# Kernel optimization log

Hardware: AMD Instinct MI355X
Metric: run time of the kernel (lower is better)

The kernel has to match this reference:

```python
import jax, jax.numpy as jnp
import numpy as np

N_KERNELS = 11
B, Q, D, E, C = 128, 32, 512, 300, 128

def _kernel_mus(n):
    mus = [1.0]
    bs = 2.0 / (n - 1)
    mus.append(1 - bs / 2)
    for i in range(1, n - 1):
        mus.append(mus[i] - bs)
    return np.array(mus, dtype=np.float32)

def _kernel_sigmas(n):
    bs = 2.0 / (n - 1)
    return np.array([0.001] + [0.5 * bs] * (n - 1), dtype=np.float32)

def setup_inputs():
    key = jax.random.key(0)
    ks = jax.random.split(key, 10)
    return {
        "query_embeddings": jax.random.normal(ks[0], (B, Q, E), jnp.float32),
        "document_embeddings": jax.random.normal(ks[1], (B, D, E), jnp.float32),
        "query_pad_oov_mask": jnp.ones((B, Q), jnp.float32),
        "document_pad_oov_mask": jnp.ones((B, D), jnp.float32),
        "conv1_w": jax.random.normal(ks[2], (C, E, 1), jnp.float32) * 0.05,
        "conv1_b": jnp.zeros((C,), jnp.float32),
        "conv2_w": jax.random.normal(ks[3], (C, E, 2), jnp.float32) * 0.05,
        "conv2_b": jnp.zeros((C,), jnp.float32),
        "conv3_w": jax.random.normal(ks[4], (C, E, 3), jnp.float32) * 0.05,
        "conv3_b": jnp.zeros((C,), jnp.float32),
        "nn_scaler": jnp.full((1,), 0.01, jnp.float32),
        "dense_w": jax.random.uniform(ks[5], (1, N_KERNELS * 9), jnp.float32, -0.014, 0.014),
        "dense_b": jnp.zeros((1,), jnp.float32),
        "dense_mean_w": jax.random.normal(ks[6], (1, N_KERNELS * 9), jnp.float32) * 0.05,
        "dense_mean_b": jnp.zeros((1,), jnp.float32),
        "dense_comb_w": jax.random.normal(ks[7], (1, 2), jnp.float32) * 0.5,
    }

def _conv_relu(x, w, b):
    # x: [B, L, E] -> [B, L, C]; right-pad by k-1 (ConstantPad1d((0, k-1))) so out len == L
    k = w.shape[-1]
    y = jax.lax.conv_general_dilated(x.transpose(0, 2, 1), w, (1,), [(0, k - 1)],
                                     dimension_numbers=("NCH", "OIH", "NCH"))
    return jax.nn.relu(y + b[None, :, None]).transpose(0, 2, 1)

def _kernel_pool(q, d, qd_mask, q_mask, doc_len, mu, sigma, scaler):
    # cosine matrix (AllenNLP CosineMatrixAttention: L2-normalize with 1e-13 tie-break)
    qn = q / (jnp.linalg.norm(q, axis=-1, keepdims=True) + 1e-13)
    dn = d / (jnp.linalg.norm(d, axis=-1, keepdims=True) + 1e-13)
    cos = jnp.einsum("bqc,bdc->bqd", qn, dn) * qd_mask
    # RBF soft-histogram kernels over the similarity matrix: [B,q,d,K]
    kr = jnp.exp(-(cos[..., None] - mu) ** 2 / (2.0 * sigma ** 2)) * qd_mask[..., None]
    pkq = kr.sum(axis=2)  # [B, Q, K]
    std = (jnp.log(jnp.clip(pkq, 1e-10)) * scaler * q_mask[..., None]).sum(axis=1)
    pkq_mean = pkq / doc_len[:, None, None]
    mean = (jnp.log(jnp.clip(pkq_mean, 1e-10)) * scaler * q_mask[..., None]).sum(axis=1)
    return std, mean

def _forward(qe, de, qm, dm, c1w, c1b, c2w, c2b, c3w, c3b, ns, dw, db, dmw, dmb, dcw):
    mu = jnp.asarray(_kernel_mus(N_KERNELS))
    sigma = jnp.asarray(_kernel_sigmas(N_KERNELS))
    qd_mask = qm[:, :, None] * dm[:, None, :]
    doc_len = dm.sum(axis=1)
    convs = [(c1w, c1b), (c2w, c2b), (c3w, c3b)]
    q_res = [_conv_relu(qe, w, b) for w, b in convs]
    d_res = [_conv_relu(de, w, b) for w, b in convs]
    std_list, mean_list = [], []
    for qr in q_res:
        for dr in d_res:
            s, m = _kernel_pool(qr, dr, qd_mask, qm, doc_len, mu, sigma, ns)
            std_list.append(s)
            mean_list.append(m)
    all_grams = jnp.concatenate(std_list, axis=1)       # [B, 9*K]
    all_grams_mean = jnp.concatenate(mean_list, axis=1)
    dense_out = all_grams @ dw.T + db
    dense_mean_out = all_grams_mean @ dmw.T + dmb
    comb = jnp.concatenate([dense_out, dense_mean_out], axis=1) @ dcw.T
    return comb[:, 0]

def reference(query_embeddings, document_embeddings, query_pad_oov_mask, document_pad_oov_mask,
              conv1_w, conv1_b, conv2_w, conv2_b, conv3_w, conv3_b,
              nn_scaler, dense_w, dense_b, dense_mean_w, dense_mean_b, dense_comb_w):
    return _forward(query_embeddings, document_embeddings, query_pad_oov_mask, document_pad_oov_mask,
                    conv1_w, conv1_b, conv2_w, conv2_b, conv3_w, conv3_b,
                    nn_scaler, dense_w, dense_b, dense_mean_w, dense_mean_b, dense_comb_w)
```

## Files before the change

kernel.cpp:

```cpp
#include <hip/hip_runtime.h>
#include <hip/hip_bf16.h>
#include <cstdint>

namespace {

typedef __bf16 bf8v __attribute__((ext_vector_type(8)));
typedef __bf16 bf4v __attribute__((ext_vector_type(4)));
typedef float  f4v  __attribute__((ext_vector_type(4)));
typedef uint32_t u32x4 __attribute__((ext_vector_type(4)));

constexpr int kB = 128;
constexpr int kQ = 32;
constexpr int kD = 512;
constexpr int kE = 300;
constexpr int kC = 128;
constexpr int kK = 11;

constexpr size_t QNB_B = 491520;
constexpr size_t DNB_B = 3637248;
constexpr size_t PKQ_B = 53968896;

constexpr float LOG2E = 1.4426950408889634f;

constexpr int XS_STRIDE = 336;

__global__ __launch_bounds__(256) void prep_kernel(
    const float* __restrict__ w1, const float* __restrict__ w2, const float* __restrict__ w3,
    __bf16* __restrict__ wb)
{
  int i = blockIdx.x * 256 + threadIdx.x;
  if (i >= 245760) return;
  int el = i & 31;
  int sc = i >> 5;
  int c  = sc & 127;
  int chunk = sc >> 7;
  int slab = chunk / 10;
  int ks = chunk - slab * 10;
  int e = ks * 32 + el;
  float v = 0.f;
  if (e < kE) {
    if (slab == 0)      v = w1[c * kE + e];
    else if (slab <= 2) v = w2[(c * kE + e) * 2 + (slab - 1)];
    else                v = w3[(c * kE + e) * 3 + (slab - 3)];
  }
  wb[i] = (__bf16)v;
}

template<int VM>
__device__ __forceinline__ void wait_vm() {
  if constexpr (VM == 4) asm volatile("s_waitcnt vmcnt(4)" ::: "memory");
  else                   asm volatile("s_waitcnt vmcnt(0)" ::: "memory");
  __builtin_amdgcn_sched_barrier(0);
}

__device__ __forceinline__ void issue4(u32x4 (&Wset)[4], const __bf16* p) {
  asm volatile("global_load_dwordx4 %0, %1, off"             : "=v"(Wset[0]) : "v"(p) : "memory");
  asm volatile("global_load_dwordx4 %0, %1, off offset:1024" : "=v"(Wset[1]) : "v"(p) : "memory");
  asm volatile("global_load_dwordx4 %0, %1, off offset:2048" : "=v"(Wset[2]) : "v"(p) : "memory");
  asm volatile("global_load_dwordx4 %0, %1, off offset:3072" : "=v"(Wset[3]) : "v"(p) : "memory");
}

__device__ __forceinline__ void mfma8(bf8v A0, bf8v A1, u32x4 (&Ws)[4], f4v (&acc)[2][4]) {
  #pragma unroll
  for (int nf = 0; nf < 4; ++nf) {
    bf8v Wf = __builtin_bit_cast(bf8v, Ws[nf]);
    acc[0][nf] = __builtin_amdgcn_mfma_f32_16x16x32_bf16(A0, Wf, acc[0][nf], 0, 0, 0);
    acc[1][nf] = __builtin_amdgcn_mfma_f32_16x16x32_bf16(A1, Wf, acc[1][nf], 0, 0, 0);
  }
}

template<int NJ, int CH0>
__device__ __forceinline__ void conv_grp(
    const __bf16* __restrict__ wb, const __bf16* __restrict__ Xs,
    int lr, int g, int wm, int wn, f4v (&acc)[2][4])
{
  const __bf16* wl = wb + (size_t)CH0 * 4096 + (wn * 64 + lr) * 32 + g * 8;
  const int arow = wm * 32 + lr;
  const int ae = g * 8;

  u32x4 W0[4], W1[4];
  issue4(W0, wl);
  issue4(W1, wl + 4096);
  const __bf16* wnext = wl + 2 * 4096;

  #pragma unroll
  for (int j = 0; j < NJ; ++j) {
    const __bf16* xr = Xs + (size_t)(arow + j) * XS_STRIDE + ae;
    const int nks = (j == NJ - 1) ? 8 : 10;
    #pragma unroll 1
    for (int ks = 0; ks < nks; ks += 2) {
      bf8v A0 = *(const bf8v*)(xr + ks * 32);
      bf8v A1 = *(const bf8v*)(xr + 16 * XS_STRIDE + ks * 32);
      wait_vm<4>();
      mfma8(A0, A1, W0, acc);
      issue4(W0, wnext); wnext += 4096;
      bf8v B0 = *(const bf8v*)(xr + ks * 32 + 32);
      bf8v B1 = *(const bf8v*)(xr + 16 * XS_STRIDE + ks * 32 + 32);
      wait_vm<4>();
      mfma8(B0, B1, W1, acc);
      issue4(W1, wnext); wnext += 4096;
    }
  }
  const __bf16* xr = Xs + (size_t)(arow + NJ - 1) * XS_STRIDE + ae;
  bf8v A0 = *(const bf8v*)(xr + 8 * 32);
  bf8v A1 = *(const bf8v*)(xr + 16 * XS_STRIDE + 8 * 32);
  wait_vm<4>();
  mfma8(A0, A1, W0, acc);
  bf8v B0 = *(const bf8v*)(xr + 9 * 32);
  bf8v B1 = *(const bf8v*)(xr + 16 * XS_STRIDE + 9 * 32);
  wait_vm<0>();
  mfma8(B0, B1, W1, acc);
}

__global__ __launch_bounds__(256, 3) void conv_fused(
    const float* __restrict__ qe, const float* __restrict__ de,
    const __bf16* __restrict__ wb,
    const float* __restrict__ b1, const float* __restrict__ b2, const float* __restrict__ b3,
    __bf16* __restrict__ qnb, __bf16* __restrict__ dnb)
{
  const int bx = blockIdx.x;
  const int b  = blockIdx.y;
  const bool isq = (bx == 0);
  const int L  = isq ? kQ : kD;
  const int p0 = isq ? 0 : (bx - 1) * 64;
  const float* xsrc = (isq ? qe : de) + (size_t)b * L * kE;

  const int t = threadIdx.x;
  const int w = t >> 6, l = t & 63;
  const int wm = w & 1, wn = w >> 1;
  const int lr = l & 15, g = l >> 4;

  __shared__ __align__(16) __bf16 Xs[66 * XS_STRIDE];
  __shared__ float sqs[2][64];

  for (int idx = t; idx < 66 * 82; idx += 256) {
    int row = idx / 82, c4 = idx - row * 82;
    int gp = p0 + row;
    float4 v = make_float4(0.f, 0.f, 0.f, 0.f);
    if (gp < L && c4 < 75) v = *(const float4*)(xsrc + (size_t)gp * kE + c4 * 4);
    bf4v hv = { (__bf16)v.x, (__bf16)v.y, (__bf16)v.z, (__bf16)v.w };
    *(bf4v*)&Xs[row * XS_STRIDE + c4 * 4] = hv;
  }
  __syncthreads();

  #pragma unroll
  for (int grp = 0; grp < 3; ++grp) {
    f4v acc[2][4];
    #pragma unroll
    for (int mf = 0; mf < 2; ++mf)
      #pragma unroll
      for (int nf = 0; nf < 4; ++nf)
        acc[mf][nf] = (f4v)0.f;

    if (grp == 0)      conv_grp<1, 0>(wb, Xs, lr, g, wm, wn, acc);
    else if (grp == 1) conv_grp<2, 10>(wb, Xs, lr, g, wm, wn, acc);
    else               conv_grp<3, 30>(wb, Xs, lr, g, wm, wn, acc);

    const float* bias = (grp == 0) ? b1 : ((grp == 1) ? b2 : b3);
    float bvs[4];
    #pragma unroll
    for (int nf = 0; nf < 4; ++nf) bvs[nf] = bias[wn * 64 + nf * 16 + lr];

    f4v ssum[2];
    #pragma unroll
    for (int mf = 0; mf < 2; ++mf) {
      ssum[mf] = (f4v)0.f;
      #pragma unroll
      for (int nf = 0; nf < 4; ++nf)
        #pragma unroll
        for (int r = 0; r < 4; ++r) {
          float y = fmaxf(acc[mf][nf][r] + bvs[nf], 0.f);
          acc[mf][nf][r] = y;
          ssum[mf][r] += y * y;
        }
    }
    #pragma unroll
    for (int off = 1; off < 16; off <<= 1)
      #pragma unroll
      for (int mf = 0; mf < 2; ++mf)
        #pragma unroll
        for (int r = 0; r < 4; ++r)
          ssum[mf][r] += __shfl_xor(ssum[mf][r], off);

    __syncthreads();
    if (lr == 0) {
      #pragma unroll
      for (int mf = 0; mf < 2; ++mf)
        *(float4*)&sqs[wn][wm * 32 + mf * 16 + g * 4] = *(float4*)&ssum[mf];
    }
    __syncthreads();
    f4v inv[2];
    #pragma unroll
    for (int mf = 0; mf < 2; ++mf) {
      float4 o = *(const float4*)&sqs[1 - wn][wm * 32 + mf * 16 + g * 4];
      inv[mf][0] = 1.f / (sqrtf(ssum[mf][0] + o.x) + 1e-13f);
      inv[mf][1] = 1.f / (sqrtf(ssum[mf][1] + o.y) + 1e-13f);
      inv[mf][2] = 1.f / (sqrtf(ssum[mf][2] + o.z) + 1e-13f);
      inv[mf][3] = 1.f / (sqrtf(ssum[mf][3] + o.w) + 1e-13f);
    }
    __syncthreads();
    __bf16* outp = (isq ? qnb : dnb) + ((size_t)(grp * kB + b)) * L * kC;
    #pragma unroll
    for (int mf = 0; mf < 2; ++mf) {
      #pragma unroll
      for (int r = 0; r < 4; ++r) {
        int gp = p0 + wm * 32 + mf * 16 + g * 4 + r;
        if (gp < L) {
          #pragma unroll
          for (int nf = 0; nf < 4; ++nf) {
            int c = wn * 64 + nf * 16 + lr;
            outp[(size_t)gp * kC + c] = (__bf16)(acc[mf][nf][r] * inv[mf][r]);
          }
        }
      }
    }
  }
}

__global__ __launch_bounds__(256) void pool_mfma(
    const __bf16* __restrict__ qnb,
    const __bf16* __restrict__ dnb,
    const float* __restrict__ qmask,
    const float* __restrict__ dmask,
    float* __restrict__ pkq)
{
  const int pair = blockIdx.x;
  const int b = blockIdx.y;
  const int qi = pair / 3, dj = pair - qi * 3;
  const __bf16* qb = qnb + ((size_t)qi * kB + b) * kQ * kC;
  const __bf16* db = dnb + ((size_t)dj * kB + b) * kD * kC;

  const int t = threadIdx.x;
  const int w = t >> 6, l = t & 63;
  const int lr = l & 15, g = l >> 4;

  __shared__ float red[4][2][16][kK];

  bf8v Bq[2][4];
  #pragma unroll
  for (int qt = 0; qt < 2; ++qt)
    #pragma unroll
    for (int kc = 0; kc < 4; ++kc)
      Bq[qt][kc] = *(const bf8v*)&qb[(size_t)(qt * 16 + lr) * kC + kc * 32 + g * 8];

  float qmv[2];
  #pragma unroll
  for (int qt = 0; qt < 2; ++qt) qmv[qt] = qmask[b * kQ + qt * 16 + lr];

  const float c1[10] = { 129.84255368f, 100.98865286f,  72.13475204f,  43.28085123f,  14.42695041f,
                         -14.42695041f, -43.28085123f, -72.13475204f, -100.98865286f, -129.84255368f };
  const float c2[10] = { -58.42914915f, -35.34602850f, -18.03368801f, -6.49212768f, -0.72134752f,
                          -0.72134752f,  -6.49212768f, -18.03368801f, -35.34602850f, -58.42914915f };
  const float C50 = -50.f * LOG2E;
  const float C0  = -500000.f * LOG2E;

  float pk[2][kK];
  #pragma unroll
  for (int qt = 0; qt < 2; ++qt)
    #pragma unroll
    for (int k = 0; k < kK; ++k) pk[qt][k] = 0.f;

  const int dt0 = w * 8;
  bf8v An[4];
  #pragma unroll
  for (int kc = 0; kc < 4; ++kc)
    An[kc] = *(const bf8v*)&db[(size_t)(dt0 * 16 + lr) * kC + kc * 32 + g * 8];

  for (int dtl = 0; dtl < 8; ++dtl) {
    const int drow0 = (dt0 + dtl) * 16;
    bf8v Ac[4];
    #pragma unroll
    for (int kc = 0; kc < 4; ++kc) Ac[kc] = An[kc];
    if (dtl < 7) {
      #pragma unroll
      for (int kc = 0; kc < 4; ++kc)
        An[kc] = *(const bf8v*)&db[(size_t)(drow0 + 16 + lr) * kC + kc * 32 + g * 8];
    }
    f4v acc0 = (f4v)0.f, acc1 = (f4v)0.f;
    #pragma unroll
    for (int kc = 0; kc < 4; ++kc) {
      acc0 = __builtin_amdgcn_mfma_f32_16x16x32_bf16(Ac[kc], Bq[0][kc], acc0, 0, 0, 0);
      acc1 = __builtin_amdgcn_mfma_f32_16x16x32_bf16(Ac[kc], Bq[1][kc], acc1, 0, 0, 0);
    }
    float4 dmv = *(const float4*)&dmask[b * kD + drow0 + g * 4];
    #pragma unroll
    for (int qt = 0; qt < 2; ++qt) {
      const f4v& a = qt ? acc1 : acc0;
      #pragma unroll
      for (int r = 0; r < 4; ++r) {
        float dm = (r == 0) ? dmv.x : (r == 1) ? dmv.y : (r == 2) ? dmv.z : dmv.w;
        float off = fmaf(dm, 1000.f, -1000.f);
        float s = a[r] * qmv[qt] * dm;
        float s2 = s * s;
        float base = fmaf(s2, C50, off);
        float dd = s - 1.f;
        pk[qt][0] += exp2f(fmaf(dd * dd, C0, off));
        #pragma unroll
        for (int k = 0; k < 10; ++k)
          pk[qt][k + 1] += exp2f(fmaf(c1[k], s, base) + c2[k]);
      }
    }
  }

  #pragma unroll
  for (int off = 16; off < 64; off <<= 1)
    #pragma unroll
    for (int qt = 0; qt < 2; ++qt)
      #pragma unroll
      for (int k = 0; k < kK; ++k)
        pk[qt][k] += __shfl_xor(pk[qt][k], off);

  if (l < 16) {
    #pragma unroll
    for (int qt = 0; qt < 2; ++qt)
      #pragma unroll
      for (int k = 0; k < kK; ++k)
        red[w][qt][lr][k] = pk[qt][k];
  }
  __syncthreads();
  for (int i = t; i < 2 * 16 * kK; i += 256) {
    int qt = i / (16 * kK);
    int rem = i - qt * 16 * kK;
    int lq = rem / kK, k = rem - lq * kK;
    float v = red[0][qt][lq][k] + red[1][qt][lq][k] + red[2][qt][lq][k] + red[3][qt][lq][k];
    int q = qt * 16 + lq;
    pkq[(((size_t)pair * kB + b) * kQ + q) * kK + k] = v * qmask[b * kQ + q];
  }
}

__global__ __launch_bounds__(128) void finalize_kernel(
    const float* __restrict__ pkq, const float* __restrict__ qmask,
    const float* __restrict__ dmask, const float* __restrict__ nsp,
    const float* __restrict__ dw, const float* __restrict__ dbp,
    const float* __restrict__ dmw, const float* __restrict__ dmbp,
    const float* __restrict__ dcw, float* __restrict__ out)
{
  const int b = blockIdx.x;
  const int t = threadIdx.x;
  __shared__ float sh[4];
  float dl = 0.f;
  for (int d = t; d < kD; d += 128) dl += dmask[b * kD + d];
  #pragma unroll
  for (int off = 1; off < 64; off <<= 1) dl += __shfl_xor(dl, off);
  if ((t & 63) == 0) sh[t >> 6] = dl;
  __syncthreads();
  const float idl = 1.f / (sh[0] + sh[1]);
  const float sc = nsp[0];
  float ps = 0.f, pm = 0.f;
  for (int i = t; i < 99; i += 128) {
    int pr = i / kK, kk = i - pr * kK;
    const float* base = pkq + ((size_t)pr * kB + b) * kQ * kK + kk;
    float ss = 0.f, sm = 0.f;
    for (int q = 0; q < kQ; ++q) {
      float v = base[q * kK];
      float qq = qmask[b * kQ + q];
      ss += __logf(fmaxf(v, 1e-10f)) * qq;
      sm += __logf(fmaxf(v * idl, 1e-10f)) * qq;
    }
    ps += dw[i] * ss;
    pm += dmw[i] * sm;
  }
  ps *= sc; pm *= sc;
  #pragma unroll
  for (int off = 1; off < 64; off <<= 1) { ps += __shfl_xor(ps, off); pm += __shfl_xor(pm, off); }
  __syncthreads();
  if ((t & 63) == 0) { sh[t >> 6] = ps; sh[2 + (t >> 6)] = pm; }
  __syncthreads();
  if (t == 0) {
    float PS = sh[0] + sh[1] + dbp[0];
    float PM = sh[2] + sh[3] + dmbp[0];
    out[b] = dcw[0] * PS + dcw[1] * PM;
  }
}

}

extern "C" void kernel_launch(void* const* d_in, const int* in_sizes, int n_in,
                              void* d_out, int out_size, void* d_ws, size_t ws_size,
                              hipStream_t stream) {
  const float* qe  = (const float*)d_in[0];
  const float* de  = (const float*)d_in[1];
  const float* qm  = (const float*)d_in[2];
  const float* dm  = (const float*)d_in[3];
  const float* w1  = (const float*)d_in[4];
  const float* b1  = (const float*)d_in[5];
  const float* w2  = (const float*)d_in[6];
  const float* b2  = (const float*)d_in[7];
  const float* w3  = (const float*)d_in[8];
  const float* b3  = (const float*)d_in[9];
  const float* ns  = (const float*)d_in[10];
  const float* dw  = (const float*)d_in[11];
  const float* db  = (const float*)d_in[12];
  const float* dmw = (const float*)d_in[13];
  const float* dmb = (const float*)d_in[14];
  const float* dcw = (const float*)d_in[15];
  float* out = (float*)d_out;

  char* wsb = (char*)d_ws;
  __bf16* wb  = (__bf16*)wsb;
  __bf16* qnb = (__bf16*)(wsb + QNB_B);
  __bf16* dnb = (__bf16*)(wsb + DNB_B);
  float*  pkq = (float*)(wsb + PKQ_B);

  prep_kernel<<<960, 256, 0, stream>>>(w1, w2, w3, wb);
  conv_fused<<<dim3(9, kB), 256, 0, stream>>>(qe, de, wb, b1, b2, b3, qnb, dnb);
  pool_mfma<<<dim3(9, kB), 256, 0, stream>>>(qnb, dnb, qm, dm, pkq);
  finalize_kernel<<<kB, 128, 0, stream>>>(pkq, qm, dm, ns, dw, db, dmw, dmb, dcw, out);
}
```

Before: 166.8 us.

## Shrink conv tile to 32 positions, staging output through LDS for coalesced stores

The conv block tile shrinks from 64 to 32 sequence positions. The four waves now split the 128 output channels as 4x32 instead of a 2x2 grid, which halves per-wave accumulators and weight registers. The grid grows to 17 blocks per batch and the occupancy hint rises from 3 to 5 blocks per CU. Normalized outputs are staged in an LDS buffer and written as 16-byte coalesced vectors instead of scattered 2-byte stores. In exchange, each block reloads the full weight set for half as many rows, which doubles global weight traffic per output.

```diff
diff --git a/kernel.cpp b/kernel.cpp
--- a/kernel.cpp
+++ b/kernel.cpp
@@ -23,6 +23,7 @@
 constexpr float LOG2E = 1.4426950408889634f;
 
 constexpr int XS_STRIDE = 336;
+constexpr int TB_STRIDE = 136;
 
 __global__ __launch_bounds__(256) void prep_kernel(
     const float* __restrict__ w1, const float* __restrict__ w2, const float* __restrict__ w3,
@@ -48,21 +49,19 @@
 
 template<int VM>
 __device__ __forceinline__ void wait_vm() {
-  if constexpr (VM == 4) asm volatile("s_waitcnt vmcnt(4)" ::: "memory");
+  if constexpr (VM == 2) asm volatile("s_waitcnt vmcnt(2)" ::: "memory");
   else                   asm volatile("s_waitcnt vmcnt(0)" ::: "memory");
   __builtin_amdgcn_sched_barrier(0);
 }
 
-__device__ __forceinline__ void issue4(u32x4 (&Wset)[4], const __bf16* p) {
+__device__ __forceinline__ void issue2(u32x4 (&Wset)[2], const __bf16* p) {
   asm volatile("global_load_dwordx4 %0, %1, off"             : "=v"(Wset[0]) : "v"(p) : "memory");
   asm volatile("global_load_dwordx4 %0, %1, off offset:1024" : "=v"(Wset[1]) : "v"(p) : "memory");
-  asm volatile("global_load_dwordx4 %0, %1, off offset:2048" : "=v"(Wset[2]) : "v"(p) : "memory");
-  asm volatile("global_load_dwordx4 %0, %1, off offset:3072" : "=v"(Wset[3]) : "v"(p) : "memory");
-}
-
-__device__ __forceinline__ void mfma8(bf8v A0, bf8v A1, u32x4 (&Ws)[4], f4v (&acc)[2][4]) {
-  #pragma unroll
-  for (int nf = 0; nf < 4; ++nf) {
+}
+
+__device__ __forceinline__ void mfma4(bf8v A0, bf8v A1, u32x4 (&Ws)[2], f4v (&acc)[2][2]) {
+  #pragma unroll
+  for (int nf = 0; nf < 2; ++nf) {
     bf8v Wf = __builtin_bit_cast(bf8v, Ws[nf]);
     acc[0][nf] = __builtin_amdgcn_mfma_f32_16x16x32_bf16(A0, Wf, acc[0][nf], 0, 0, 0);
     acc[1][nf] = __builtin_amdgcn_mfma_f32_16x16x32_bf16(A1, Wf, acc[1][nf], 0, 0, 0);
@@ -72,47 +71,46 @@
 template<int NJ, int CH0>
 __device__ __forceinline__ void conv_grp(
     const __bf16* __restrict__ wb, const __bf16* __restrict__ Xs,
-    int lr, int g, int wm, int wn, f4v (&acc)[2][4])
+    int w, int lr, int g, f4v (&acc)[2][2])
 {
-  const __bf16* wl = wb + (size_t)CH0 * 4096 + (wn * 64 + lr) * 32 + g * 8;
-  const int arow = wm * 32 + lr;
+  const __bf16* wl = wb + (size_t)CH0 * 4096 + (w * 32 + lr) * 32 + g * 8;
   const int ae = g * 8;
 
-  u32x4 W0[4], W1[4];
-  issue4(W0, wl);
-  issue4(W1, wl + 4096);
+  u32x4 W0[2], W1[2];
+  issue2(W0, wl);
+  issue2(W1, wl + 4096);
   const __bf16* wnext = wl + 2 * 4096;
 
   #pragma unroll
   for (int j = 0; j < NJ; ++j) {
-    const __bf16* xr = Xs + (size_t)(arow + j) * XS_STRIDE + ae;
+    const __bf16* xr = Xs + (size_t)(lr + j) * XS_STRIDE + ae;
     const int nks = (j == NJ - 1) ? 8 : 10;
     #pragma unroll 1
     for (int ks = 0; ks < nks; ks += 2) {
       bf8v A0 = *(const bf8v*)(xr + ks * 32);
       bf8v A1 = *(const bf8v*)(xr + 16 * XS_STRIDE + ks * 32);
-      wait_vm<4>();
-      mfma8(A0, A1, W0, acc);
-      issue4(W0, wnext); wnext += 4096;
+      wait_vm<2>();
+      mfma4(A0, A1, W0, acc);
+      issue2(W0, wnext); wnext += 4096;
       bf8v B0 = *(const bf8v*)(xr + ks * 32 + 32);
       bf8v B1 = *(const bf8v*)(xr + 16 * XS_STRIDE + ks * 32 + 32);
-      wait_vm<4>();
-      mfma8(B0, B1, W1, acc);
-      issue4(W1, wnext); wnext += 4096;
-    }
-  }
-  const __bf16* xr = Xs + (size_t)(arow + NJ - 1) * XS_STRIDE + ae;
+      wait_vm<2>();
+      mfma4(B0, B1, W1, acc);
+      issue2(W1, wnext); wnext += 4096;
+    }
+  }
+  const __bf16* xr = Xs + (size_t)(lr + NJ - 1) * XS_STRIDE + ae;
   bf8v A0 = *(const bf8v*)(xr + 8 * 32);
   bf8v A1 = *(const bf8v*)(xr + 16 * XS_STRIDE + 8 * 32);
-  wait_vm<4>();
-  mfma8(A0, A1, W0, acc);
+  wait_vm<2>();
+  mfma4(A0, A1, W0, acc);
   bf8v B0 = *(const bf8v*)(xr + 9 * 32);
   bf8v B1 = *(const bf8v*)(xr + 16 * XS_STRIDE + 9 * 32);
   wait_vm<0>();
-  mfma8(B0, B1, W1, acc);
-}
-
-__global__ __launch_bounds__(256, 3) void conv_fused(
+  mfma4(B0, B1, W1, acc);
+}
+
+__global__ __launch_bounds__(256, 5) void conv_fused(
     const float* __restrict__ qe, const float* __restrict__ de,
     const __bf16* __restrict__ wb,
     const float* __restrict__ b1, const float* __restrict__ b2, const float* __restrict__ b3,
@@ -122,18 +120,18 @@
   const int b  = blockIdx.y;
   const bool isq = (bx == 0);
   const int L  = isq ? kQ : kD;
-  const int p0 = isq ? 0 : (bx - 1) * 64;
+  const int p0 = isq ? 0 : (bx - 1) * 32;
   const float* xsrc = (isq ? qe : de) + (size_t)b * L * kE;
 
   const int t = threadIdx.x;
   const int w = t >> 6, l = t & 63;
-  const int wm = w & 1, wn = w >> 1;
   const int lr = l & 15, g = l >> 4;
 
-  __shared__ __align__(16) __bf16 Xs[66 * XS_STRIDE];
-  __shared__ float sqs[2][64];
-
-  for (int idx = t; idx < 66 * 82; idx += 256) {
+  __shared__ __align__(16) __bf16 Xs[34 * XS_STRIDE];
+  __shared__ __align__(16) __bf16 tbuf[32 * TB_STRIDE];
+  __shared__ float sqs4[4][32];
+
+  for (int idx = t; idx < 34 * 82; idx += 256) {
     int row = idx / 82, c4 = idx - row * 82;
     int gp = p0 + row;
     float4 v = make_float4(0.f, 0.f, 0.f, 0.f);
@@ -145,28 +143,28 @@
 
   #pragma unroll
   for (int grp = 0; grp < 3; ++grp) {
-    f4v acc[2][4];
+    f4v acc[2][2];
     #pragma unroll
     for (int mf = 0; mf < 2; ++mf)
       #pragma unroll
-      for (int nf = 0; nf < 4; ++nf)
+      for (int nf = 0; nf < 2; ++nf)
         acc[mf][nf] = (f4v)0.f;
 
-    if (grp == 0)      conv_grp<1, 0>(wb, Xs, lr, g, wm, wn, acc);
-    else if (grp == 1) conv_grp<2, 10>(wb, Xs, lr, g, wm, wn, acc);
-    else               conv_grp<3, 30>(wb, Xs, lr, g, wm, wn, acc);
+    if (grp == 0)      conv_grp<1, 0>(wb, Xs, w, lr, g, acc);
+    else if (grp == 1) conv_grp<2, 10>(wb, Xs, w, lr, g, acc);
+    else               conv_grp<3, 30>(wb, Xs, w, lr, g, acc);
 
     const float* bias = (grp == 0) ? b1 : ((grp == 1) ? b2 : b3);
-    float bvs[4];
-    #pragma unroll
-    for (int nf = 0; nf < 4; ++nf) bvs[nf] = bias[wn * 64 + nf * 16 + lr];
+    float bvs[2];
+    #pragma unroll
+    for (int nf = 0; nf < 2; ++nf) bvs[nf] = bias[w * 32 + nf * 16 + lr];
 
     f4v ssum[2];
     #pragma unroll
     for (int mf = 0; mf < 2; ++mf) {
       ssum[mf] = (f4v)0.f;
       #pragma unroll
-      for (int nf = 0; nf < 4; ++nf)
+      for (int nf = 0; nf < 2; ++nf)
         #pragma unroll
         for (int r = 0; r < 4; ++r) {
           float y = fmaxf(acc[mf][nf][r] + bvs[nf], 0.f);
@@ -182,38 +180,40 @@
         for (int r = 0; r < 4; ++r)
           ssum[mf][r] += __shfl_xor(ssum[mf][r], off);
 
+    if (lr == 0) {
+      #pragma unroll
+      for (int mf = 0; mf < 2; ++mf)
+        *(float4*)&sqs4[w][mf * 16 + g * 4] = *(float4*)&ssum[mf];
+    }
     __syncthreads();
-    if (lr == 0) {
-      #pragma unroll
-      for (int mf = 0; mf < 2; ++mf)
-        *(float4*)&sqs[wn][wm * 32 + mf * 16 + g * 4] = *(float4*)&ssum[mf];
-    }
+    float inv[2][4];
+    #pragma unroll
+    for (int mf = 0; mf < 2; ++mf)
+      #pragma unroll
+      for (int r = 0; r < 4; ++r) {
+        int row = mf * 16 + g * 4 + r;
+        float s = sqs4[0][row] + sqs4[1][row] + sqs4[2][row] + sqs4[3][row];
+        inv[mf][r] = 1.f / (sqrtf(s) + 1e-13f);
+      }
+    #pragma unroll
+    for (int mf = 0; mf < 2; ++mf)
+      #pragma unroll
+      for (int nf = 0; nf < 2; ++nf)
+        #pragma unroll
+        for (int r = 0; r < 4; ++r) {
+          int row = mf * 16 + g * 4 + r;
+          int c = w * 32 + nf * 16 + lr;
+          tbuf[row * TB_STRIDE + c] = (__bf16)(acc[mf][nf][r] * inv[mf][r]);
+        }
     __syncthreads();
-    f4v inv[2];
-    #pragma unroll
-    for (int mf = 0; mf < 2; ++mf) {
-      float4 o = *(const float4*)&sqs[1 - wn][wm * 32 + mf * 16 + g * 4];
-      inv[mf][0] = 1.f / (sqrtf(ssum[mf][0] + o.x) + 1e-13f);
-      inv[mf][1] = 1.f / (sqrtf(ssum[mf][1] + o.y) + 1e-13f);
-      inv[mf][2] = 1.f / (sqrtf(ssum[mf][2] + o.z) + 1e-13f);
-      inv[mf][3] = 1.f / (sqrtf(ssum[mf][3] + o.w) + 1e-13f);
-    }
+    __bf16* outp = (isq ? qnb : dnb) + ((size_t)(grp * kB + b)) * L * kC + (size_t)p0 * kC;
+    #pragma unroll
+    for (int ci = t; ci < 512; ci += 256) {
+      bf8v v = *(const bf8v*)&tbuf[(ci >> 4) * TB_STRIDE + (ci & 15) * 8];
+      *(bf8v*)(outp + ci * 8) = v;
+    }
+    asm volatile("s_waitcnt vmcnt(0)" ::: "memory");
     __syncthreads();
-    __bf16* outp = (isq ? qnb : dnb) + ((size_t)(grp * kB + b)) * L * kC;
-    #pragma unroll
-    for (int mf = 0; mf < 2; ++mf) {
-      #pragma unroll
-      for (int r = 0; r < 4; ++r) {
-        int gp = p0 + wm * 32 + mf * 16 + g * 4 + r;
-        if (gp < L) {
-          #pragma unroll
-          for (int nf = 0; nf < 4; ++nf) {
-            int c = wn * 64 + nf * 16 + lr;
-            outp[(size_t)gp * kC + c] = (__bf16)(acc[mf][nf][r] * inv[mf][r]);
-          }
-        }
-      }
-    }
   }
 }
 
@@ -403,7 +403,7 @@
   float*  pkq = (float*)(wsb + PKQ_B);
 
   prep_kernel<<<960, 256, 0, stream>>>(w1, w2, w3, wb);
-  conv_fused<<<dim3(9, kB), 256, 0, stream>>>(qe, de, wb, b1, b2, b3, qnb, dnb);
+  conv_fused<<<dim3(17, kB), 256, 0, stream>>>(qe, de, wb, b1, b2, b3, qnb, dnb);
   pool_mfma<<<dim3(9, kB), 256, 0, stream>>>(qnb, dnb, qm, dm, pkq);
   finalize_kernel<<<kB, 128, 0, stream>>>(pkq, qm, dm, ns, dw, db, dmw, dmb, dcw, out);
 }
```

Result: faster. 162.7 us (-2.5%).
